# Kernel optimization log

Measured on AMD Instinct MI355X. Metric: run time of the kernel, lower is better.

## Reference

```python
import jax, jax.numpy as jnp
import numpy as np

N = 50000          # nodes
E = 800000         # edges (before self loops)
G = 64             # graphs in batch
HEADS = 4
HID = 25
DENSE = HEADS * HID      # 100, must equal prototype feature dim
IN_DIM = 128
OUT_DIM = 2
NPC = 5                  # num_prototypes_per_class
NUM_PROT = OUT_DIM * NPC
EPS = 1e-4
NEG_SLOPE = 0.2


def setup_inputs() -> dict:
    key = jax.random.key(0)
    ks = jax.random.split(key, 20)
    x = jax.random.normal(ks[0], (N, IN_DIM), dtype=jnp.float32)
    edge_index = jax.random.randint(ks[1], (2, E), 0, N, dtype=jnp.int64)
    batch = jnp.sort(jax.random.randint(ks[2], (N,), 0, G, dtype=jnp.int64))
    inp = {"x": x, "edge_index": edge_index, "batch": batch}
    in_dims = [IN_DIM, DENSE, DENSE]
    for i in range(3):
        d = in_dims[i]
        s = 1.0 / np.sqrt(d)
        inp[f"W{i}"] = jax.random.uniform(ks[3 + 4 * i], (d, DENSE), jnp.float32, -s, s)
        inp[f"as{i}"] = jax.random.uniform(ks[4 + 4 * i], (HEADS, HID), jnp.float32, -s, s)
        inp[f"ad{i}"] = jax.random.uniform(ks[5 + 4 * i], (HEADS, HID), jnp.float32, -s, s)
        inp[f"b{i}"] = jnp.zeros((DENSE,), jnp.float32)
    inp["protos"] = jax.random.uniform(ks[16], (NUM_PROT, DENSE), jnp.float32)
    # last_layer weight: +1 for own class, -0.5 otherwise  [OUT_DIM, NUM_PROT]
    cls = jnp.arange(NUM_PROT) // NPC
    inp["last_w"] = jnp.where(cls[None, :] == jnp.arange(OUT_DIM)[:, None], 1.0, -0.5).astype(jnp.float32)
    return inp


def _gat_layer(x, src, dst, W, a_src, a_dst, b):
    h = (x @ W).reshape(N, HEADS, HID)                 # [N,H,D]
    e_src = jnp.einsum('nhd,hd->nh', h, a_src)         # [N,H]
    e_dst = jnp.einsum('nhd,hd->nh', h, a_dst)
    alpha = e_src[src] + e_dst[dst]                    # [Etot,H]
    alpha = jnp.where(alpha > 0, alpha, NEG_SLOPE * alpha)
    amax = jax.ops.segment_max(alpha, dst, num_segments=N)
    ex = jnp.exp(alpha - amax[dst])
    denom = jax.ops.segment_sum(ex, dst, num_segments=N)
    a = ex / (denom[dst] + 1e-16)                      # segmented softmax over in-edges
    msg = h[src] * a[:, :, None]                       # [Etot,H,D]
    out = jax.ops.segment_sum(msg, dst, num_segments=N)
    return out.reshape(N, DENSE) + b


def reference(x, edge_index, batch, W0, as0, ad0, b0, W1, as1, ad1, b1, W2, as2, ad2, b2, protos, last_w):
    loops = jnp.arange(N, dtype=edge_index.dtype)
    src = jnp.concatenate([edge_index[0], loops])      # PyG add_self_loops=True
    dst = jnp.concatenate([edge_index[1], loops])
    params = [(W0, as0, ad0, b0), (W1, as1, ad1, b1), (W2, as2, ad2, b2)]
    h = x
    for (W, a_s, a_d, b) in params:
        h = _gat_layer(h, src, dst, W, a_s, a_d, b)
        h = jax.nn.relu(h)
    node_emb = h
    graph_emb = jax.ops.segment_max(h, batch, num_segments=G)   # global_max_pool
    # prototype distances: squared euclidean via expansion
    xp = graph_emb @ protos.T                                    # [G,P]
    dist = -2.0 * xp + jnp.sum(graph_emb ** 2, axis=1, keepdims=True) + jnp.sum(protos ** 2, axis=1)[None, :]
    sim = jnp.log((dist + 1.0) / (dist + EPS))
    logits = sim @ last_w.T
    probs = jax.nn.softmax(logits, axis=-1)
    return logits, probs, node_emb, graph_emb, dist
```

## Files before the change

kernel.cpp:

```cpp
#include <hip/hip_runtime.h>
#include <hip/hip_bf16.h>

#define NN      50000
#define EE      800000
#define ETOT    (EE + NN)
#define GG      64
#define HEADS   4
#define HID     25
#define DENSE   100
#define IN_DIM  128
#define OUT_DIM 2
#define NPC     5
#define NUM_PROT (OUT_DIM * NPC)
#define NCHUNK  ((NN + 255) / 256)

#define NEG_INF (-3.402823466e38f)

__global__ void k_count(const int* __restrict__ ei, int* __restrict__ cnt, int* __restrict__ pos) {
    int e = blockIdx.x * blockDim.x + threadIdx.x;
    if (e >= ETOT) return;
    int dst = (e < EE) ? ei[EE + e] : (e - EE);
    pos[e] = atomicAdd(&cnt[dst], 1);
}

__global__ void k_scan1(const int* __restrict__ cnt, int* __restrict__ csum) {
    __shared__ int sh[256];
    int i = blockIdx.x * 256 + threadIdx.x;
    int v = (i < NN) ? cnt[i] : 0;
    sh[threadIdx.x] = v;
    __syncthreads();
    for (int s = 128; s > 0; s >>= 1) {
        if (threadIdx.x < s) sh[threadIdx.x] += sh[threadIdx.x + s];
        __syncthreads();
    }
    if (threadIdx.x == 0) csum[blockIdx.x] = sh[0];
}

__global__ void k_scan2(int* __restrict__ csum) {
    __shared__ int sh[256];
    int tid = threadIdx.x;
    int v = (tid < NCHUNK) ? csum[tid] : 0;
    sh[tid] = v;
    __syncthreads();
    for (int s = 1; s < 256; s <<= 1) {
        int t = (tid >= s) ? sh[tid - s] : 0;
        __syncthreads();
        sh[tid] += t;
        __syncthreads();
    }
    if (tid < NCHUNK) csum[tid] = sh[tid] - v;
    if (tid == NCHUNK) csum[NCHUNK] = sh[255];
}

__global__ void k_scan3(const int* __restrict__ cnt, const int* __restrict__ csum, int* __restrict__ offs) {
    __shared__ int sh[256];
    int i = blockIdx.x * 256 + threadIdx.x;
    int v = (i < NN) ? cnt[i] : 0;
    sh[threadIdx.x] = v;
    __syncthreads();
    for (int s = 1; s < 256; s <<= 1) {
        int t = (threadIdx.x >= s) ? sh[threadIdx.x - s] : 0;
        __syncthreads();
        sh[threadIdx.x] += t;
        __syncthreads();
    }
    int excl = sh[threadIdx.x] - v + csum[blockIdx.x];
    if (i <= NN) offs[i] = excl;
}

__global__ void k_scatter(const int* __restrict__ ei, const int* __restrict__ offs,
                          const int* __restrict__ pos, int* __restrict__ csr) {
    int e = blockIdx.x * blockDim.x + threadIdx.x;
    if (e >= ETOT) return;
    int src, dst;
    if (e < EE) { src = ei[e]; dst = ei[EE + e]; }
    else        { src = dst = e - EE; }
    csr[offs[dst] + pos[e]] = src;
}

__global__ void k_bounds(const int* __restrict__ batch, int* __restrict__ gstart) {
    int n = blockIdx.x * blockDim.x + threadIdx.x;
    if (n >= NN) return;
    int b = batch[n];
    if (n == 0) {
        for (int g = 0; g <= b; g++) gstart[g] = 0;
    } else {
        int pb = batch[n - 1];
        for (int g = pb + 1; g <= b; g++) gstart[g] = n;
    }
    if (n == NN - 1) {
        for (int g = b + 1; g <= GG; g++) gstart[g] = NN;
    }
}

template <int DIN, int KC>
__global__ __launch_bounds__(256) void k_gemm(const float* __restrict__ X,
                                              const float* __restrict__ W,
                                              float* __restrict__ H) {
    __shared__ float Ws[KC * 104];
    __shared__ float Xs[32 * (KC + 1)];
    const int tid = threadIdx.x;
    const int rl = tid >> 5;
    const int cg = tid & 31;
    const int node0 = blockIdx.x * 32;

    float acc[4][4] = {};
    constexpr int NCH = DIN / KC;
    for (int kb = 0; kb < NCH; ++kb) {
        const int k0 = kb * KC;
        for (int idx = tid; idx < KC * 100; idx += 256) {
            int k = idx / 100, c = idx - k * 100;
            Ws[k * 104 + c] = W[(k0 + k) * 100 + c];
        }
        for (int idx = tid; idx < 32 * KC; idx += 256) {
            int r = idx / KC, k = idx - r * KC;
            int row = node0 + r;
            Xs[r * (KC + 1) + k] = (row < NN) ? X[(size_t)row * DIN + k0 + k] : 0.f;
        }
        __syncthreads();
        if (cg < 25) {
            #pragma unroll
            for (int k = 0; k < KC; ++k) {
                float4 w = *reinterpret_cast<const float4*>(&Ws[k * 104 + cg * 4]);
                #pragma unroll
                for (int j = 0; j < 4; ++j) {
                    float xv = Xs[(rl + 8 * j) * (KC + 1) + k];
                    acc[j][0] += xv * w.x; acc[j][1] += xv * w.y;
                    acc[j][2] += xv * w.z; acc[j][3] += xv * w.w;
                }
            }
        }
        __syncthreads();
    }
    if (cg < 25) {
        #pragma unroll
        for (int j = 0; j < 4; ++j) {
            int row = node0 + rl + 8 * j;
            if (row < NN) {
                float4 v = {acc[j][0], acc[j][1], acc[j][2], acc[j][3]};
                *reinterpret_cast<float4*>(&H[(size_t)row * 100 + cg * 4]) = v;
            }
        }
    }
}

__global__ void k_esed(const float* __restrict__ H, const float* __restrict__ AS,
                       const float* __restrict__ AD, float* __restrict__ es, float* __restrict__ ed) {
    int t = blockIdx.x * blockDim.x + threadIdx.x;
    if (t >= NN * HEADS) return;
    int n = t >> 2, hd = t & 3;
    const float* hr = H + (size_t)n * 100 + hd * 25;
    const float* as = AS + hd * 25;
    const float* ad = AD + hd * 25;
    float s1 = 0.f, s2 = 0.f;
    #pragma unroll
    for (int d = 0; d < 25; d++) {
        float v = hr[d];
        s1 += v * as[d];
        s2 += v * ad[d];
    }
    es[t] = s1;
    ed[t] = s2;
}

__global__ __launch_bounds__(256) void k_msum(const float* __restrict__ es,
                                              const float* __restrict__ ed,
                                              const int* __restrict__ offs,
                                              const int* __restrict__ csr,
                                              float* __restrict__ wv) {
    int wid = threadIdx.x >> 6;
    int lane = threadIdx.x & 63;
    int n = blockIdx.x * 4 + wid;
    if (n >= NN) return;
    int el = lane >> 2, hd = lane & 3;
    int beg = offs[n], end = offs[n + 1];
    float edh = ed[n * 4 + hd];
    float m = NEG_INF, s = 0.f;
    for (int e = beg + el; e < end; e += 16) {
        int si = csr[e];
        float a = es[si * 4 + hd] + edh;
        a = (a > 0.f) ? a : 0.2f * a;
        float nm = fmaxf(m, a);
        float sc = __expf(m - nm);
        s = s * sc + __expf(a - nm);
        m = nm;
    }
    #pragma unroll
    for (int mask = 4; mask <= 32; mask <<= 1) {
        float mo = __shfl_xor(m, mask, 64);
        float so = __shfl_xor(s, mask, 64);
        float nm = fmaxf(m, mo);
        float f1 = (m  > NEG_INF) ? __expf(m  - nm) : 0.f;
        float f2 = (mo > NEG_INF) ? __expf(mo - nm) : 0.f;
        s = s * f1 + so * f2;
        m = nm;
    }
    float invs = 1.f / (s + 1e-16f);
    for (int e = beg + el; e < end; e += 16) {
        int si = csr[e];
        float a = es[si * 4 + hd] + edh;
        a = (a > 0.f) ? a : 0.2f * a;
        wv[(size_t)e * 4 + hd] = __expf(a - m) * invs;
    }
}

__global__ __launch_bounds__(128) void k_acc(const float* __restrict__ H,
                                             const float* __restrict__ wv,
                                             const int* __restrict__ offs,
                                             const int* __restrict__ csr,
                                             const float* __restrict__ bias,
                                             float* __restrict__ out) {
    int wid = threadIdx.x >> 6;
    int lane = threadIdx.x & 63;
    int n = blockIdx.x * 2 + wid;
    if (n >= NN || lane >= 50) return;
    int d0 = lane * 2;
    int h0 = d0 / 25, h1 = (d0 + 1) / 25;
    int beg = offs[n], end = offs[n + 1];
    float ax = 0.f, ay = 0.f;
    int e = beg;
    for (; e + 4 <= end; e += 4) {
        int s0 = csr[e], s1 = csr[e + 1], s2 = csr[e + 2], s3 = csr[e + 3];
        float2 x0 = *reinterpret_cast<const float2*>(&H[(size_t)s0 * 100 + d0]);
        float2 x1 = *reinterpret_cast<const float2*>(&H[(size_t)s1 * 100 + d0]);
        float2 x2 = *reinterpret_cast<const float2*>(&H[(size_t)s2 * 100 + d0]);
        float2 x3 = *reinterpret_cast<const float2*>(&H[(size_t)s3 * 100 + d0]);
        float w0x = wv[(size_t)e * 4 + h0],       w0y = wv[(size_t)e * 4 + h1];
        float w1x = wv[(size_t)(e + 1) * 4 + h0], w1y = wv[(size_t)(e + 1) * 4 + h1];
        float w2x = wv[(size_t)(e + 2) * 4 + h0], w2y = wv[(size_t)(e + 2) * 4 + h1];
        float w3x = wv[(size_t)(e + 3) * 4 + h0], w3y = wv[(size_t)(e + 3) * 4 + h1];
        ax += w0x * x0.x; ay += w0y * x0.y;
        ax += w1x * x1.x; ay += w1y * x1.y;
        ax += w2x * x2.x; ay += w2y * x2.y;
        ax += w3x * x3.x; ay += w3y * x3.y;
    }
    for (; e < end; ++e) {
        float2 xv = *reinterpret_cast<const float2*>(&H[(size_t)csr[e] * 100 + d0]);
        ax += wv[(size_t)e * 4 + h0] * xv.x;
        ay += wv[(size_t)e * 4 + h1] * xv.y;
    }
    float2 b = *reinterpret_cast<const float2*>(&bias[d0]);
    float2 o = {fmaxf(ax + b.x, 0.f), fmaxf(ay + b.y, 0.f)};
    *reinterpret_cast<float2*>(&out[(size_t)n * 100 + d0]) = o;
}

__global__ void k_pool1(const float* __restrict__ NE, const int* __restrict__ gstart,
                        float* __restrict__ part) {
    int g = blockIdx.x >> 3, c = blockIdx.x & 7;
    int d = threadIdx.x;
    if (d >= 100) return;
    int s0 = gstart[g], s1 = gstart[g + 1];
    int len = s1 - s0;
    int n0 = s0 + (int)((long long)len * c / 8);
    int n1 = s0 + (int)((long long)len * (c + 1) / 8);
    float vm = NEG_INF;
    for (int n = n0; n < n1; n++) vm = fmaxf(vm, NE[(size_t)n * 100 + d]);
    part[(size_t)(g * 8 + c) * 100 + d] = vm;
}

__global__ void k_pool2(const float* __restrict__ part, float* __restrict__ GE) {
    int g = blockIdx.x;
    int d = threadIdx.x;
    if (d >= 100) return;
    float vm = NEG_INF;
    for (int c = 0; c < 8; c++) vm = fmaxf(vm, part[(size_t)(g * 8 + c) * 100 + d]);
    GE[(size_t)g * 100 + d] = vm;
}

__global__ void k_head(const float* __restrict__ GE, const float* __restrict__ P,
                       const float* __restrict__ LW, float* __restrict__ logits,
                       float* __restrict__ probs, float* __restrict__ dist) {
    int g = blockIdx.x;
    __shared__ float ge[100];
    __shared__ float sims[NUM_PROT];
    __shared__ float lg[OUT_DIM];
    int t = threadIdx.x;
    if (t < 100) ge[t] = GE[(size_t)g * 100 + t];
    __syncthreads();
    if (t < NUM_PROT) {
        float dot = 0.f, pn = 0.f, gn = 0.f;
        for (int d = 0; d < 100; d++) {
            float pv = P[t * 100 + d];
            float gv = ge[d];
            dot += gv * pv;
            pn += pv * pv;
            gn += gv * gv;
        }
        float ds = gn - 2.f * dot + pn;
        dist[g * NUM_PROT + t] = ds;
        sims[t] = logf((ds + 1.f) / (ds + 1e-4f));
    }
    __syncthreads();
    if (t < OUT_DIM) {
        float l = 0.f;
        for (int p = 0; p < NUM_PROT; p++) l += sims[p] * LW[t * NUM_PROT + p];
        lg[t] = l;
        logits[g * OUT_DIM + t] = l;
    }
    __syncthreads();
    if (t == 0) {
        float mm = fmaxf(lg[0], lg[1]);
        float e0 = __expf(lg[0] - mm), e1 = __expf(lg[1] - mm);
        float inv = 1.f / (e0 + e1);
        probs[g * OUT_DIM + 0] = e0 * inv;
        probs[g * OUT_DIM + 1] = e1 * inv;
    }
}

extern "C" void kernel_launch(void* const* d_in, const int* in_sizes, int n_in,
                              void* d_out, int out_size, void* d_ws, size_t ws_size,
                              hipStream_t stream) {
    const float* x     = (const float*)d_in[0];
    const int*   ei    = (const int*)d_in[1];
    const int*   batch = (const int*)d_in[2];
    const float* Wm[3]  = {(const float*)d_in[3],  (const float*)d_in[7],  (const float*)d_in[11]};
    const float* ASm[3] = {(const float*)d_in[4],  (const float*)d_in[8],  (const float*)d_in[12]};
    const float* ADm[3] = {(const float*)d_in[5],  (const float*)d_in[9],  (const float*)d_in[13]};
    const float* Bm[3]  = {(const float*)d_in[6],  (const float*)d_in[10], (const float*)d_in[14]};
    const float* P  = (const float*)d_in[15];
    const float* LW = (const float*)d_in[16];

    float* out = (float*)d_out;
    float* logits  = out;
    float* probs   = out + GG * OUT_DIM;
    float* nodeEmb = out + 2 * GG * OUT_DIM;
    float* GE      = nodeEmb + (size_t)NN * DENSE;
    float* disto   = GE + GG * DENSE;

    char* w = (char*)d_ws;
    size_t off = 0;
    auto carve = [&](size_t bytes) -> void* {
        void* p = w + off;
        off += (bytes + 15) & ~(size_t)15;
        return p;
    };
    float* hA   = (float*)carve((size_t)NN * DENSE * 4);
    float* es   = (float*)carve((size_t)NN * HEADS * 4);
    float* ed   = (float*)carve((size_t)NN * HEADS * 4);
    int* cnt    = (int*)carve((size_t)NN * 4);
    int* offs   = (int*)carve((size_t)(NN + 1) * 4);
    int* pos    = (int*)carve((size_t)ETOT * 4);
    int* csr    = (int*)carve((size_t)ETOT * 4);
    int* csum   = (int*)carve((size_t)(NCHUNK + 1) * 4);
    int* gstart = (int*)carve((size_t)(GG + 1) * 4);
    float* part = (float*)carve((size_t)GG * 8 * DENSE * 4);
    float* wv   = (float*)carve((size_t)ETOT * HEADS * 4);
    bool has_wv = (off <= ws_size);
    (void)in_sizes; (void)n_in; (void)out_size;

    hipMemsetAsync(cnt, 0, (size_t)NN * 4, stream);
    k_count<<<(ETOT + 255) / 256, 256, 0, stream>>>(ei, cnt, pos);
    k_scan1<<<NCHUNK, 256, 0, stream>>>(cnt, csum);
    k_scan2<<<1, 256, 0, stream>>>(csum);
    k_scan3<<<NCHUNK, 256, 0, stream>>>(cnt, csum, offs);
    k_scatter<<<(ETOT + 255) / 256, 256, 0, stream>>>(ei, offs, pos, csr);
    k_bounds<<<(NN + 255) / 256, 256, 0, stream>>>(batch, gstart);

    const int gemmGrid = (NN + 31) / 32;
    const int esedGrid = (NN * HEADS + 255) / 256;
    const int msumGrid = (NN + 3) / 4;
    const int accGrid  = (NN + 1) / 2;

    const float* layerIn = x;
    for (int l = 0; l < 3; ++l) {
        if (l == 0) k_gemm<IN_DIM, 32><<<gemmGrid, 256, 0, stream>>>(layerIn, Wm[l], hA);
        else        k_gemm<DENSE,  25><<<gemmGrid, 256, 0, stream>>>(layerIn, Wm[l], hA);
        k_esed<<<esedGrid, 256, 0, stream>>>(hA, ASm[l], ADm[l], es, ed);
        k_msum<<<msumGrid, 256, 0, stream>>>(es, ed, offs, csr, wv);
        k_acc<<<accGrid, 128, 0, stream>>>(hA, wv, offs, csr, Bm[l], nodeEmb);
        layerIn = nodeEmb;
        (void)has_wv;
    }

    k_pool1<<<GG * 8, 128, 0, stream>>>(nodeEmb, gstart, part);
    k_pool2<<<GG, 128, 0, stream>>>(part, GE);

    k_head<<<GG, 128, 0, stream>>>(GE, P, LW, logits, probs, disto);
}
```

Baseline: 483.6 us.

## Enlarge GEMM tile to 128 rows with float4 loads; unroll gather by 8

The node-feature GEMM now handles 128 rows per block. Each thread accumulates 16 rows, and X is staged into shared memory with float4 loads and read back as float4 along k. This raises arithmetic reuse of the W tile and cuts shared-memory loads per FMA, at the cost of many more registers and fewer blocks. The k_acc gather loop is also reworked into an 8-wide unrolled body with clamped, zero-weighted tail handling so more loads are in flight per iteration.

```diff
diff --git a/kernel.cpp b/kernel.cpp
--- a/kernel.cpp
+++ b/kernel.cpp
@@ -97,36 +97,48 @@
 __global__ __launch_bounds__(256) void k_gemm(const float* __restrict__ X,
                                               const float* __restrict__ W,
                                               float* __restrict__ H) {
+    constexpr int XSTR = KC + 4;
     __shared__ float Ws[KC * 104];
-    __shared__ float Xs[32 * (KC + 1)];
+    __shared__ float Xs[128 * XSTR];
     const int tid = threadIdx.x;
     const int rl = tid >> 5;
     const int cg = tid & 31;
-    const int node0 = blockIdx.x * 32;
-
-    float acc[4][4] = {};
+    const int node0 = blockIdx.x * 128;
+
+    float acc[16][4] = {};
     constexpr int NCH = DIN / KC;
+    constexpr int KQ = KC / 4;
     for (int kb = 0; kb < NCH; ++kb) {
         const int k0 = kb * KC;
         for (int idx = tid; idx < KC * 100; idx += 256) {
             int k = idx / 100, c = idx - k * 100;
             Ws[k * 104 + c] = W[(k0 + k) * 100 + c];
         }
-        for (int idx = tid; idx < 32 * KC; idx += 256) {
-            int r = idx / KC, k = idx - r * KC;
+        for (int q = tid; q < 128 * KQ; q += 256) {
+            int r = q / KQ, kq = q - r * KQ;
             int row = node0 + r;
-            Xs[r * (KC + 1) + k] = (row < NN) ? X[(size_t)row * DIN + k0 + k] : 0.f;
+            float4 v = {0.f, 0.f, 0.f, 0.f};
+            if (row < NN) v = *reinterpret_cast<const float4*>(&X[(size_t)row * DIN + k0 + kq * 4]);
+            *reinterpret_cast<float4*>(&Xs[r * XSTR + kq * 4]) = v;
         }
         __syncthreads();
         if (cg < 25) {
-            #pragma unroll
-            for (int k = 0; k < KC; ++k) {
-                float4 w = *reinterpret_cast<const float4*>(&Ws[k * 104 + cg * 4]);
+            for (int kq = 0; kq < KQ; ++kq) {
+                float4 w0 = *reinterpret_cast<const float4*>(&Ws[(kq * 4 + 0) * 104 + cg * 4]);
+                float4 w1 = *reinterpret_cast<const float4*>(&Ws[(kq * 4 + 1) * 104 + cg * 4]);
+                float4 w2 = *reinterpret_cast<const float4*>(&Ws[(kq * 4 + 2) * 104 + cg * 4]);
+                float4 w3 = *reinterpret_cast<const float4*>(&Ws[(kq * 4 + 3) * 104 + cg * 4]);
                 #pragma unroll
-                for (int j = 0; j < 4; ++j) {
-                    float xv = Xs[(rl + 8 * j) * (KC + 1) + k];
-                    acc[j][0] += xv * w.x; acc[j][1] += xv * w.y;
-                    acc[j][2] += xv * w.z; acc[j][3] += xv * w.w;
+                for (int j = 0; j < 16; ++j) {
+                    float4 xv = *reinterpret_cast<const float4*>(&Xs[(rl * 16 + j) * XSTR + kq * 4]);
+                    acc[j][0] += xv.x * w0.x; acc[j][1] += xv.x * w0.y;
+                    acc[j][2] += xv.x * w0.z; acc[j][3] += xv.x * w0.w;
+                    acc[j][0] += xv.y * w1.x; acc[j][1] += xv.y * w1.y;
+                    acc[j][2] += xv.y * w1.z; acc[j][3] += xv.y * w1.w;
+                    acc[j][0] += xv.z * w2.x; acc[j][1] += xv.z * w2.y;
+                    acc[j][2] += xv.z * w2.z; acc[j][3] += xv.z * w2.w;
+                    acc[j][0] += xv.w * w3.x; acc[j][1] += xv.w * w3.y;
+                    acc[j][2] += xv.w * w3.z; acc[j][3] += xv.w * w3.w;
                 }
             }
         }
@@ -134,8 +146,8 @@
     }
     if (cg < 25) {
         #pragma unroll
-        for (int j = 0; j < 4; ++j) {
-            int row = node0 + rl + 8 * j;
+        for (int j = 0; j < 16; ++j) {
+            int row = node0 + rl * 16 + j;
             if (row < NN) {
                 float4 v = {acc[j][0], acc[j][1], acc[j][2], acc[j][3]};
                 *reinterpret_cast<float4*>(&H[(size_t)row * 100 + cg * 4]) = v;
@@ -218,26 +230,19 @@
     int h0 = d0 / 25, h1 = (d0 + 1) / 25;
     int beg = offs[n], end = offs[n + 1];
     float ax = 0.f, ay = 0.f;
-    int e = beg;
-    for (; e + 4 <= end; e += 4) {
-        int s0 = csr[e], s1 = csr[e + 1], s2 = csr[e + 2], s3 = csr[e + 3];
-        float2 x0 = *reinterpret_cast<const float2*>(&H[(size_t)s0 * 100 + d0]);
-        float2 x1 = *reinterpret_cast<const float2*>(&H[(size_t)s1 * 100 + d0]);
-        float2 x2 = *reinterpret_cast<const float2*>(&H[(size_t)s2 * 100 + d0]);
-        float2 x3 = *reinterpret_cast<const float2*>(&H[(size_t)s3 * 100 + d0]);
-        float w0x = wv[(size_t)e * 4 + h0],       w0y = wv[(size_t)e * 4 + h1];
-        float w1x = wv[(size_t)(e + 1) * 4 + h0], w1y = wv[(size_t)(e + 1) * 4 + h1];
-        float w2x = wv[(size_t)(e + 2) * 4 + h0], w2y = wv[(size_t)(e + 2) * 4 + h1];
-        float w3x = wv[(size_t)(e + 3) * 4 + h0], w3y = wv[(size_t)(e + 3) * 4 + h1];
-        ax += w0x * x0.x; ay += w0y * x0.y;
-        ax += w1x * x1.x; ay += w1y * x1.y;
-        ax += w2x * x2.x; ay += w2y * x2.y;
-        ax += w3x * x3.x; ay += w3y * x3.y;
-    }
-    for (; e < end; ++e) {
-        float2 xv = *reinterpret_cast<const float2*>(&H[(size_t)csr[e] * 100 + d0]);
-        ax += wv[(size_t)e * 4 + h0] * xv.x;
-        ay += wv[(size_t)e * 4 + h1] * xv.y;
+    for (int e = beg; e < end; e += 8) {
+        #pragma unroll
+        for (int u = 0; u < 8; ++u) {
+            int ee = e + u;
+            int ec = (ee < end) ? ee : beg;
+            int idx = csr[ec];
+            float wx = wv[(size_t)ec * 4 + h0];
+            float wy = wv[(size_t)ec * 4 + h1];
+            if (ee >= end) { wx = 0.f; wy = 0.f; }
+            float2 xv = *reinterpret_cast<const float2*>(&H[(size_t)idx * 100 + d0]);
+            ax += wx * xv.x;
+            ay += wy * xv.y;
+        }
     }
     float2 b = *reinterpret_cast<const float2*>(&bias[d0]);
     float2 o = {fmaxf(ax + b.x, 0.f), fmaxf(ay + b.y, 0.f)};
@@ -345,8 +350,7 @@
     int* gstart = (int*)carve((size_t)(GG + 1) * 4);
     float* part = (float*)carve((size_t)GG * 8 * DENSE * 4);
     float* wv   = (float*)carve((size_t)ETOT * HEADS * 4);
-    bool has_wv = (off <= ws_size);
-    (void)in_sizes; (void)n_in; (void)out_size;
+    (void)in_sizes; (void)n_in; (void)out_size; (void)ws_size;
 
     hipMemsetAsync(cnt, 0, (size_t)NN * 4, stream);
     k_count<<<(ETOT + 255) / 256, 256, 0, stream>>>(ei, cnt, pos);
@@ -356,7 +360,7 @@
     k_scatter<<<(ETOT + 255) / 256, 256, 0, stream>>>(ei, offs, pos, csr);
     k_bounds<<<(NN + 255) / 256, 256, 0, stream>>>(batch, gstart);
 
-    const int gemmGrid = (NN + 31) / 32;
+    const int gemmGrid = (NN + 127) / 128;
     const int esedGrid = (NN * HEADS + 255) / 256;
     const int msumGrid = (NN + 3) / 4;
     const int accGrid  = (NN + 1) / 2;
@@ -364,12 +368,11 @@
     const float* layerIn = x;
     for (int l = 0; l < 3; ++l) {
         if (l == 0) k_gemm<IN_DIM, 32><<<gemmGrid, 256, 0, stream>>>(layerIn, Wm[l], hA);
-        else        k_gemm<DENSE,  25><<<gemmGrid, 256, 0, stream>>>(layerIn, Wm[l], hA);
+        else        k_gemm<DENSE,  20><<<gemmGrid, 256, 0, stream>>>(layerIn, Wm[l], hA);
         k_esed<<<esedGrid, 256, 0, stream>>>(hA, ASm[l], ADm[l], es, ed);
         k_msum<<<msumGrid, 256, 0, stream>>>(es, ed, offs, csr, wv);
         k_acc<<<accGrid, 128, 0, stream>>>(hA, wv, offs, csr, Bm[l], nodeEmb);
         layerIn = nodeEmb;
-        (void)has_wv;
     }
 
     k_pool1<<<GG * 8, 128, 0, stream>>>(nodeEmb, gstart, part);
```

Measured after the change: 457.7 us. 5.3% less time.
